# Kernel tuning notes

Measured on AMD Instinct MI355X. Metric: run time of the kernel, lower is better.

The kernel has to match this reference:

```python
import jax, jax.numpy as jnp
import numpy as np

B, L, D = 512, 200, 128
N_ITEMS = 50001
T_STEPS = 4
TAU = 2.0
STEP = 1
V_TH = 1.0
SG_ALPHA = 4.0  # spikingjelly default surrogate.Sigmoid alpha


@jax.custom_vjp
def spike(x):
    return (x >= 0.0).astype(x.dtype)

def _spike_fwd(x):
    return spike(x), x

def _spike_bwd(x, g):
    s = jax.nn.sigmoid(SG_ALPHA * x)
    return (g * SG_ALPHA * s * (1.0 - s),)

spike.defvjp(_spike_fwd, _spike_bwd)


def lif_multistep(x):
    """Multi-step LIF (hard reset to 0, detach_reset). x: [T, ...] -> spikes [T, ...]."""
    def step(v, xt):
        v = v + (xt - v) / TAU  # charge (v_reset = 0)
        s = spike(v - V_TH)
        v = v - jax.lax.stop_gradient(s) * v  # hard reset, detached spike
        return v, s
    v0 = jnp.zeros_like(x[0])
    _, spikes = jax.lax.scan(step, v0, x)
    return spikes


def layernorm(x, g, b, eps=1e-5):
    m = x.mean(-1, keepdims=True)
    v = x.var(-1, keepdims=True)
    return (x - m) / jnp.sqrt(v + eps) * g + b


def _build_session_graphs(rng):
    lens = rng.integers(50, L + 1, size=B)
    item_seq = np.zeros((B, L), dtype=np.int64)
    for b in range(B):
        item_seq[b, :lens[b]] = rng.integers(1, N_ITEMS, size=lens[b])
    alias = np.zeros((B, L), dtype=np.int64)
    items = np.zeros((B, L), dtype=np.int64)
    A = np.zeros((B, L, 2 * L), dtype=np.float32)
    for b in range(B):
        u = item_seq[b]
        node = np.unique(u)  # sorted
        items[b, :len(node)] = node
        alias[b] = np.searchsorted(node, u)
        uA = np.zeros((L, L), dtype=np.float32)
        for i in range(L - 1):
            if u[i + 1] == 0:
                break
            r = np.searchsorted(node, u[i])
            c = np.searchsorted(node, u[i + 1])
            uA[r, c] = 1.0
        sin = uA.sum(0); sin[sin == 0] = 1.0
        sout = uA.sum(1); sout[sout == 0] = 1.0
        A[b, :, :L] = (uA / sin).T          # u_A_in.T
        A[b, :, L:] = ((uA.T / sout)).T     # u_A_out.T
    mask = item_seq > 0
    return A, alias, items, mask, lens.astype(np.int64)


def setup_inputs() -> dict:
    rng = np.random.default_rng(0)
    A, alias, items, mask, lens = _build_session_graphs(rng)
    stdv = 1.0 / np.sqrt(D)
    key = jax.random.key(0)
    ks = jax.random.split(key, 24)
    u = lambda k, shape: jax.random.uniform(k, shape, jnp.float32, -stdv, stdv)
    item_emb = u(ks[0], (N_ITEMS, D)).at[0].set(0.0)  # padding_idx=0
    return {
        "A": jnp.asarray(A),
        "alias_inputs": jnp.asarray(alias),
        "items": jnp.asarray(items),
        "mask": jnp.asarray(mask),
        "item_seq_len": jnp.asarray(lens),
        "item_emb": item_emb,
        "W_in": u(ks[1], (D, D)), "b_in": u(ks[2], (D,)),
        "W_out": u(ks[3], (D, D)), "b_out": u(ks[4], (D,)),
        "w_ih": u(ks[5], (3 * D, 2 * D)), "w_hh": u(ks[6], (3 * D, D)),
        "b_ih": u(ks[7], (3 * D,)), "b_hh": u(ks[8], (3 * D,)),
        "b_iah": u(ks[9], (D,)), "b_ioh": u(ks[10], (D,)),
        "W1": u(ks[11], (D, D)), "W2": u(ks[12], (D, D)),
        "W3": u(ks[13], (1, D)), "Wt": u(ks[14], (D, 2 * D)),
        "g_q": u(ks[15], (D,)), "beta_q": u(ks[16], (D,)),
        "g_sh": u(ks[17], (2 * D,)), "beta_sh": u(ks[18], (2 * D,)),
    }


def _forward(A, alias_inputs, items, mask, item_seq_len, item_emb,
             W_in, b_in, W_out, b_out, w_ih, w_hh, b_ih, b_hh, b_iah, b_ioh,
             W1, W2, W3, Wt, g_q, beta_q, g_sh, beta_sh):
    hidden = item_emb[items]  # [B,L,D]
    for _ in range(STEP):
        ein = hidden @ W_in.T + b_in
        eout = hidden @ W_out.T + b_out
        input_in = jnp.einsum('bij,bjd->bid', A[:, :, :L], ein) + b_iah
        input_out = jnp.einsum('bij,bjd->bid', A[:, :, L:], eout) + b_ioh
        inputs = jnp.concatenate([input_in, input_out], axis=-1)  # [B,L,2D]
        gi = inputs @ w_ih.T + b_ih  # [B,L,3D]
        gh = hidden @ w_hh.T + b_hh
        i_r, i_i, i_n = jnp.split(gi, 3, axis=-1)
        h_r, h_i, h_n = jnp.split(gh, 3, axis=-1)
        r = jax.nn.sigmoid(i_r + h_r)
        z = jax.nn.sigmoid(i_i + h_i)
        n = jnp.tanh(i_n + r * h_n)
        hidden = (1.0 - z) * hidden + z * n
    seq_hidden = jnp.take_along_axis(hidden, alias_inputs[..., None], axis=1)  # [B,L,D]
    ht = jnp.take_along_axis(seq_hidden, (item_seq_len - 1)[:, None, None], axis=1)[:, 0]  # [B,D]
    Qb = (ht @ W1.T)[:, None, :] + seq_hidden @ W2.T  # [B,L,D]
    Q = jnp.broadcast_to(Qb[None], (T_STEPS, B, L, D))
    Qs = lif_multistep(layernorm(Q, g_q, beta_q))
    alpha = Qs @ W3.T  # [T,B,L,1]
    mf = mask.astype(alpha.dtype)
    a = jnp.sum(alpha * seq_hidden[None] * mf[None, :, :, None], axis=2)  # [T,B,D]
    ht_T = jnp.broadcast_to(ht[None], (T_STEPS, B, D))
    sh = jnp.concatenate([a, ht_T], axis=-1)  # [T,B,2D]
    sh = layernorm(lif_multistep(sh), g_sh, beta_sh)
    return (sh @ Wt.T).mean(0)  # [B,D]


def reference(A, alias_inputs, items, mask, item_seq_len, item_emb,
              W_in, b_in, W_out, b_out, w_ih, w_hh, b_ih, b_hh, b_iah, b_ioh,
              W1, W2, W3, Wt, g_q, beta_q, g_sh, beta_sh):
    return _forward(A, alias_inputs, items, mask, item_seq_len, item_emb,
                    W_in, b_in, W_out, b_out, w_ih, w_hh, b_ih, b_hh, b_iah, b_ioh,
                    W1, W2, W3, Wt, g_q, beta_q, g_sh, beta_sh)
```

## Files before the change

### kernel.cpp

```cpp
#include <hip/hip_runtime.h>
#include <hip/hip_bf16.h>
#include <cstdint>
#include <cstddef>

#define B_ 512
#define L_ 200
#define D_ 128
#define M_ (B_*L_)
#define T_ 4

typedef short bf16x8 __attribute__((ext_vector_type(8)));
typedef unsigned short u16x8 __attribute__((ext_vector_type(8)));
typedef float f32x4 __attribute__((ext_vector_type(4)));

__device__ __forceinline__ float bf2f(unsigned short u){
  union { unsigned int i; float f; } c; c.i = ((unsigned int)u)<<16; return c.f;
}
__device__ __forceinline__ unsigned short f2bf(float f){
  union { float f; unsigned int i; } c; c.f = f;
  unsigned int r = c.i + 0x7FFFu + ((c.i>>16)&1u);
  return (unsigned short)(r>>16);
}
__device__ __forceinline__ float wsum(float v){
  #pragma unroll
  for (int m=1;m<64;m<<=1) v += __shfl_xor(v, m, 64);
  return v;
}
__device__ __forceinline__ void gload_lds16(const void* g, void* l){
  __builtin_amdgcn_global_load_lds(
      (const __attribute__((address_space(1))) void*)g,
      (__attribute__((address_space(3))) void*)l, 16, 0, 0);
}

__global__ __launch_bounds__(256)
void gemm_bt(const unsigned short* __restrict__ A, int lda,
             const unsigned short* __restrict__ Bt, int ldb,
             const float* __restrict__ bias,
             unsigned short* __restrict__ C, int ldc, int K,
             const int* __restrict__ mlimit)
{
  const int m0 = blockIdx.y * 128;
  if (mlimit && m0 >= *mlimit) return;
  __shared__ __align__(16) short sAs[2][128*32];
  __shared__ __align__(16) short sBs[2][128*32];
  const int tid = threadIdx.x;
  const int n0 = blockIdx.x * 128;
  const int lane = tid & 63;
  const int w = tid >> 6;
  const int wr = (w>>1)*64, wc = (w&1)*64;

  f32x4 acc[4][4];
  #pragma unroll
  for (int i=0;i<4;i++)
    #pragma unroll
    for (int j=0;j<4;j++) acc[i][j] = (f32x4){0.f,0.f,0.f,0.f};

  const int c1 = tid, c2 = tid + 256;
  const int r1 = c1>>2, s1 = c1&3, k1 = ((s1 ^ ((r1>>1)&3))&3)<<3;
  const int r2 = c2>>2, s2 = c2&3, k2 = ((s2 ^ ((r2>>1)&3))&3)<<3;
  const int fr = lane & 15;
  const int fq = lane >> 4;
  const int fk = ((fq ^ ((fr>>1)&3))&3)<<3;

  auto stage = [&](int t){
    const int buf = t & 1, ks = t << 5;
    gload_lds16(A  + (size_t)(m0 + r1)*lda + ks + k1, sAs[buf] + (size_t)c1*8);
    gload_lds16(A  + (size_t)(m0 + r2)*lda + ks + k2, sAs[buf] + (size_t)c2*8);
    gload_lds16(Bt + (size_t)(n0 + r1)*ldb + ks + k1, sBs[buf] + (size_t)c1*8);
    gload_lds16(Bt + (size_t)(n0 + r2)*ldb + ks + k2, sBs[buf] + (size_t)c2*8);
  };
  const int nT = K >> 5;
  stage(0);
  __syncthreads();
  for (int t=0; t<nT; ++t){
    if (t+1 < nT) stage(t+1);
    const short* a_ = sAs[t&1];
    const short* b_ = sBs[t&1];
    bf16x8 af[4], bfr[4];
    #pragma unroll
    for (int i=0;i<4;i++){
      af[i]  = *(const bf16x8*)(a_ + (wr + i*16 + fr)*32 + fk);
      bfr[i] = *(const bf16x8*)(b_ + (wc + i*16 + fr)*32 + fk);
    }
    #pragma unroll
    for (int i=0;i<4;i++)
      #pragma unroll
      for (int j=0;j<4;j++)
        acc[i][j] = __builtin_amdgcn_mfma_f32_16x16x32_bf16(af[i], bfr[j], acc[i][j], 0,0,0);
    __syncthreads();
  }

  const int orow = fq<<2;
  #pragma unroll
  for (int i=0;i<4;i++){
    #pragma unroll
    for (int j=0;j<4;j++){
      const int gn = n0 + wc + j*16 + fr;
      const float bv = bias ? bias[gn] : 0.f;
      #pragma unroll
      for (int v=0;v<4;v++){
        const int gm = m0 + wr + i*16 + orow + v;
        C[(size_t)gm*ldc + gn] = f2bf(acc[i][j][v] + bv);
      }
    }
  }
}

__global__ __launch_bounds__(128)
void k_prepW(const float* __restrict__ w_ih, const float* __restrict__ w_hh,
             const float* __restrict__ W_in, const float* __restrict__ W_out,
             const float* __restrict__ b_in, const float* __restrict__ b_out,
             const float* __restrict__ b_ih, const float* __restrict__ b_hh,
             const float* __restrict__ b_iah, const float* __restrict__ b_ioh,
             const float* __restrict__ W2,
             unsigned short* __restrict__ Wbig, float* __restrict__ biasBase,
             float* __restrict__ uIn, float* __restrict__ uOut,
             unsigned short* __restrict__ w2b)
{
  const int p = blockIdx.x, t = threadIdx.x;
  if (p < 128) w2b[p*128 + t] = f2bf(W2[p*128 + t]);
  const int dim = p>>2, g = p&3;
  const int row = (g==0) ? dim : (g==1) ? 128+dim : 256+dim;
  const bool has_ih = (g!=3), has_hh = (g!=2);
  __shared__ float wl[128], wrg[128], red[3][128];
  wl[t]  = has_ih ? w_ih[(size_t)row*256 + t]       : 0.f;
  wrg[t] = has_ih ? w_ih[(size_t)row*256 + 128 + t] : 0.f;
  __syncthreads();
  float cin = 0.f, cout = 0.f;
  if (has_ih) {
    for (int m=0;m<128;m++){
      cin  += wl[m]  * W_in [m*128 + t];
      cout += wrg[m] * W_out[m*128 + t];
    }
  }
  Wbig[(size_t)p*384 +       t] = f2bf(cin);
  Wbig[(size_t)p*384 + 128 + t] = f2bf(cout);
  Wbig[(size_t)p*384 + 256 + t] = f2bf(has_hh ? w_hh[(size_t)row*128 + t] : 0.f);
  red[0][t] = wl[t]*b_iah[t] + wrg[t]*b_ioh[t];
  red[1][t] = wl[t]*b_in[t];
  red[2][t] = wrg[t]*b_out[t];
  __syncthreads();
  if (t == 0) {
    float v=0.f, ui=0.f, uo=0.f;
    for (int k=0;k<128;k++){ v += red[0][k]; ui += red[1][k]; uo += red[2][k]; }
    float bb;
    if (g==0)      bb = b_ih[dim]     + b_hh[dim]     + v;
    else if (g==1) bb = b_ih[128+dim] + b_hh[128+dim] + v;
    else if (g==2) bb = b_ih[256+dim] + v;
    else           bb = b_hh[256+dim];
    biasBase[p] = bb;
    uIn[p]  = has_ih ? ui : 0.f;
    uOut[p] = has_ih ? uo : 0.f;
  }
}

__global__ __launch_bounds__(64)
void k_nb(const int* __restrict__ alias, const int* __restrict__ lens,
          int* __restrict__ nb)
{
  const int b = blockIdx.x, lane = threadIdx.x;
  const int len = lens[b];
  int m = 0;
  for (int l=lane; l<len; l+=64) m = max(m, alias[b*L_ + l]);
  #pragma unroll
  for (int o=1;o<64;o<<=1) m = max(m, __shfl_xor(m, o, 64));
  if (lane==0) nb[b] = m + 1;
}

__global__ __launch_bounds__(512)
void k_scan(const int* __restrict__ nb, const int* __restrict__ lens,
            int* __restrict__ nbase, int* __restrict__ vbase)
{
  __shared__ int A[2][512], Bv[2][512];
  const int t = threadIdx.x;
  const int a0 = nb[t], b0 = lens[t];
  A[0][t] = a0; Bv[0][t] = b0;
  __syncthreads();
  int cur = 0;
  for (int off=1; off<512; off<<=1){
    const int nxt = cur^1;
    A[nxt][t]  = A[cur][t]  + (t>=off ? A[cur][t-off]  : 0);
    Bv[nxt][t] = Bv[cur][t] + (t>=off ? Bv[cur][t-off] : 0);
    __syncthreads();
    cur = nxt;
  }
  nbase[t] = A[cur][t] - a0;
  vbase[t] = Bv[cur][t] - b0;
  if (t==511){ nbase[512] = A[cur][511]; vbase[512] = Bv[cur][511]; }
}

__global__ __launch_bounds__(1024)
void k_aggemb(const int* __restrict__ alias, const int* __restrict__ items,
              const int* __restrict__ lens, const float* __restrict__ emb,
              const int* __restrict__ nb, const int* __restrict__ nbase,
              unsigned short* __restrict__ X3, unsigned char* __restrict__ cf)
{
  const int b = blockIdx.x, tid = threadIdx.x;
  __shared__ unsigned short hl[L_*128];
  __shared__ int al[L_], it[L_];
  __shared__ unsigned bmIn[L_*8], bmOut[L_*8];
  if (tid < L_) { al[tid] = alias[b*L_ + tid]; it[tid] = items[b*L_ + tid]; }
  for (int i=tid; i<L_*8; i+=1024){ bmIn[i]=0u; bmOut[i]=0u; }
  __syncthreads();
  const int len = lens[b], nB = nb[b], base = nbase[b];
  if (tid < len-1) {
    const int r = al[tid], c = al[tid+1];
    atomicOr(&bmIn[c*8 + (r>>5)],  1u<<(r&31));
    atomicOr(&bmOut[r*8 + (c>>5)], 1u<<(c&31));
  }
  const int rr = tid>>5, cc = (tid&31)<<2;
  for (int s=0; s<nB; s+=32) {
    const int j = s + rr;
    if (j < nB) {
      const float4 v = *(const float4*)(emb + (size_t)it[j]*128 + cc);
      ushort4 o; o.x=f2bf(v.x); o.y=f2bf(v.y); o.z=f2bf(v.z); o.w=f2bf(v.w);
      *(ushort4*)(hl + j*128 + cc) = o;
      *(ushort4*)(X3 + (size_t)(base + j)*384 + 256 + cc) = o;
    }
  }
  __syncthreads();
  const int g = tid >> 7, d = tid & 127;
  for (int s=0; s<nB; s+=8) {
    const int i = s + g;
    if (i < nB) {
      float si=0.f, so=0.f; int ci=0, co=0;
      #pragma unroll
      for (int wd=0; wd<8; ++wd) {
        unsigned word = bmIn[i*8+wd];
        while (word) { int j = __ffs(word)-1; word &= word-1u;
          si += bf2f(hl[(wd*32+j)*128 + d]); ci++; }
        word = bmOut[i*8+wd];
        while (word) { int j = __ffs(word)-1; word &= word-1u;
          so += bf2f(hl[(wd*32+j)*128 + d]); co++; }
      }
      unsigned short* xr = X3 + (size_t)(base + i)*384;
      xr[d]       = f2bf(si / (float)(ci>0?ci:1));
      xr[128 + d] = f2bf(so / (float)(co>0?co:1));
      if (d == 0) cf[base + i] = (unsigned char)((ci>0?1:0) | (co>0?2:0));
    }
  }
}

__global__ __launch_bounds__(512)
void k_gates_gru(const unsigned short* __restrict__ X3,
                 const unsigned short* __restrict__ Wbig,
                 const float* __restrict__ biasBase,
                 const float* __restrict__ uIn,
                 const float* __restrict__ uOut,
                 const unsigned char* __restrict__ cf,
                 unsigned short* __restrict__ hidden,
                 const int* __restrict__ mlimit)
{
  const int m0 = blockIdx.y * 128;
  if (m0 >= *mlimit) return;
  __shared__ __align__(16) short sA[2][128*32];
  __shared__ __align__(16) short sB[2][256*32];
  const int tid = threadIdx.x;
  const int p0 = blockIdx.x * 256;
  const int lane = tid & 63;
  const int w = tid >> 6;
  const int wr  = (w>>2)*64;
  const int wcp = (w&3)*64;
  const int fr = lane & 15;
  const int fq = lane >> 4;
  const int fk = ((fq ^ ((fr>>1)&3))&3)<<3;

  f32x4 acc[4][4];
  #pragma unroll
  for (int i=0;i<4;i++)
    #pragma unroll
    for (int j=0;j<4;j++) acc[i][j] = (f32x4){0.f,0.f,0.f,0.f};

  const int ra = tid>>2, sa_ = tid&3, ka = ((sa_ ^ ((ra>>1)&3))&3)<<3;
  const int c1 = tid + 512, rb1 = c1>>2, sb1 = c1&3, kb1 = ((sb1 ^ ((rb1>>1)&3))&3)<<3;

  auto stage = [&](int t){
    const int buf = t & 1, ks = t << 5;
    gload_lds16(X3   + (size_t)(m0 + ra )*384 + ks + ka , sA[buf] + (size_t)tid*8);
    gload_lds16(Wbig + (size_t)(p0 + ra )*384 + ks + ka , sB[buf] + (size_t)tid*8);
    gload_lds16(Wbig + (size_t)(p0 + rb1)*384 + ks + kb1, sB[buf] + (size_t)(c1-512)*8 + 512*8);
  };
  stage(0);
  __syncthreads();
  for (int t=0; t<12; ++t){
    if (t < 11) stage(t+1);
    const short* a_ = sA[t&1];
    const short* b_ = sB[t&1];
    bf16x8 af[4], bfr[4];
    #pragma unroll
    for (int i=0;i<4;i++){
      af[i]  = *(const bf16x8*)(a_ + (wr  + i*16 + fr)*32 + fk);
      bfr[i] = *(const bf16x8*)(b_ + (wcp + i*16 + fr)*32 + fk);
    }
    #pragma unroll
    for (int i=0;i<4;i++)
      #pragma unroll
      for (int j=0;j<4;j++)
        acc[i][j] = __builtin_amdgcn_mfma_f32_16x16x32_bf16(af[i], bfr[j], acc[i][j], 0,0,0);
    __syncthreads();
  }

  const bool q0b = (lane & 1), q1b = (lane & 2);
  #pragma unroll
  for (int j=0;j<4;j++){
    const int dim = (p0>>2) + (w&3)*16 + j*4 + ((lane>>2)&3);
    const float4 bb = *(const float4*)(biasBase + dim*4);
    const float4 bi = *(const float4*)(uIn  + dim*4);
    const float4 bo = *(const float4*)(uOut + dim*4);
    #pragma unroll
    for (int i=0;i<4;i++){
      const float a0=acc[i][j][0], a1=acc[i][j][1], a2=acc[i][j][2], a3=acc[i][j][3];
      const float t0=__shfl_xor(a0,1), t1=__shfl_xor(a1,1), t2=__shfl_xor(a2,1), t3=__shfl_xor(a3,1);
      const float s0 = q0b? t1:a0, s1 = q0b? a1:t0, s2 = q0b? t3:a2, s3 = q0b? a3:t2;
      const float u0=__shfl_xor(s0,2), u1=__shfl_xor(s1,2), u2=__shfl_xor(s2,2), u3=__shfl_xor(s3,2);
      float G0 = q1b? u2:s0, G1 = q1b? u3:s1, G2 = q1b? s2:u0, G3 = q1b? s3:u1;
      const int row = m0 + wr + i*16 + fq*4 + (lane&3);
      const unsigned c = cf[row];
      const float fi = (c&1) ? 1.f : 0.f, fo = (c&2) ? 1.f : 0.f;
      G0 += bb.x + fi*bi.x + fo*bo.x;
      G1 += bb.y + fi*bi.y + fo*bo.y;
      G2 += bb.z + fi*bi.z + fo*bo.z;
      G3 += bb.w;
      const float h = bf2f(X3[(size_t)row*384 + 256 + dim]);
      const float r = 1.f/(1.f+__expf(-G0));
      const float z = 1.f/(1.f+__expf(-G1));
      const float x = G2 + r*G3;
      const float n = 1.f - 2.f/(__expf(2.f*x)+1.f);
      hidden[(size_t)row*128 + dim] = f2bf((1.f-z)*h + z*n);
    }
  }
}

__global__ __launch_bounds__(256)
void k_gather(const unsigned short* __restrict__ hidden,
              const int* __restrict__ alias, const int* __restrict__ lens,
              const int* __restrict__ nbase, const int* __restrict__ vbase,
              unsigned short* __restrict__ seqv)
{
  const int idx = blockIdx.x*256 + threadIdx.x;
  const int row = idx >> 4, d8 = (idx & 15) << 3;
  const int b = row / L_, l = row - b*L_;
  const int len = lens[b];
  if (l >= len) return;
  const int vrow = vbase[b] + l;
  u16x8 v = *(const u16x8*)(hidden + (size_t)(nbase[b] + alias[row])*128 + d8);
  *(u16x8*)(seqv + (size_t)vrow*128 + d8) = v;
}

__global__ __launch_bounds__(1024)
void k_attn(const unsigned short* __restrict__ Q0,
            const unsigned short* __restrict__ seqv, const int* __restrict__ lens,
            const int* __restrict__ vbase, const float* __restrict__ W1,
            const float* __restrict__ g_q, const float* __restrict__ beta_q,
            const float* __restrict__ W3, float* __restrict__ a_out)
{
  const int b = blockIdx.x, tid = threadIdx.x;
  const int w = tid>>6, lane = tid&63;
  __shared__ float a_acc[16][T_][128];
  __shared__ float htv[128], htw[128];
  const int len = lens[b], vb = vbase[b];
  for (int i=tid; i<16*T_*128; i+=1024) ((float*)a_acc)[i] = 0.f;
  if (tid < 128) htv[tid] = bf2f(seqv[(size_t)(vb + len - 1)*128 + tid]);
  __syncthreads();
  {
    const int d = tid >> 3, seg = (tid & 7) << 4;
    const float* wr1 = W1 + (size_t)d*128 + seg;
    const float* hv = htv + seg;
    float p = 0.f;
    #pragma unroll
    for (int k=0;k<16;k++) p += wr1[k]*hv[k];
    p += __shfl_xor(p, 1, 64); p += __shfl_xor(p, 2, 64); p += __shfl_xor(p, 4, 64);
    if ((tid & 7) == 0) htw[d] = p;
  }
  __syncthreads();
  const float h0 = htw[lane], h1 = htw[lane+64];
  const float gq0 = g_q[lane], gq1 = g_q[lane+64];
  const float bq0 = beta_q[lane], bq1 = beta_q[lane+64];
  const float w30 = W3[lane], w31 = W3[lane+64];
  for (int l = w; l < len; l += 16) {
    const size_t row = (size_t)(vb + l);
    const float q0 = bf2f(Q0[row*128 + lane]) + h0;
    const float q1 = bf2f(Q0[row*128 + lane + 64]) + h1;
    const float m = wsum(q0+q1) * (1.f/128.f);
    const float d0 = q0-m, d1 = q1-m;
    const float var = wsum(d0*d0 + d1*d1) * (1.f/128.f);
    const float inv = rsqrtf(var + 1e-5f);
    const float x0 = d0*inv*gq0 + bq0;
    const float x1 = d1*inv*gq1 + bq1;
    const float sh0 = bf2f(seqv[row*128+lane]), sh1 = bf2f(seqv[row*128+lane+64]);
    float v0=0.f, v1=0.f;
    #pragma unroll
    for (int t=0;t<T_;t++){
      v0 = 0.5f*(v0+x0); v1 = 0.5f*(v1+x1);
      const float s0 = (v0>=1.f)?1.f:0.f, s1 = (v1>=1.f)?1.f:0.f;
      v0 -= s0*v0; v1 -= s1*v1;
      const float alpha = wsum(s0*w30 + s1*w31);
      a_acc[w][t][lane] += alpha*sh0; a_acc[w][t][lane+64] += alpha*sh1;
    }
  }
  __syncthreads();
  for (int i=tid; i<T_*128; i+=1024){
    const int t = i>>7, d = i&127;
    float s = 0.f;
    #pragma unroll
    for (int p=0;p<16;p++) s += a_acc[p][t][d];
    a_out[((size_t)t*B_ + b)*128 + d] = s;
  }
}

__global__ __launch_bounds__(256)
void k_final(const float* __restrict__ a_in, const unsigned short* __restrict__ hidden,
             const int* __restrict__ alias, const int* __restrict__ lens,
             const int* __restrict__ nbase,
             const float* __restrict__ g_sh, const float* __restrict__ beta_sh,
             const float* __restrict__ Wt, float* __restrict__ out)
{
  const int b = blockIdx.x, tid = threadIdx.x;
  const int w = tid>>6, lane = tid&63;
  __shared__ float ys[256];
  __shared__ float part[T_][4];
  const int len = lens[b];
  float xh = 0.f;
  if (tid >= 128) {
    const int al = alias[b*L_ + len - 1];
    xh = bf2f(hidden[((size_t)(nbase[b] + al))*128 + (tid-128)]);
  }
  float v = 0.f; float sp[T_];
  #pragma unroll
  for (int t=0;t<T_;t++){
    const float x = (tid<128) ? a_in[((size_t)t*B_ + b)*128 + tid] : xh;
    v = 0.5f*(v + x);
    const float s = (v>=1.f)?1.f:0.f;
    v -= s*v;
    sp[t] = s;
  }
  #pragma unroll
  for (int t=0;t<T_;t++){
    const float r = wsum(sp[t]);
    if (lane==0) part[t][w] = r;
  }
  __syncthreads();
  float acc4 = 0.f;
  #pragma unroll
  for (int t=0;t<T_;t++){
    const float k = part[t][0]+part[t][1]+part[t][2]+part[t][3];
    const float mean = k * (1.f/256.f);
    const float varr = mean - mean*mean;
    const float inv = rsqrtf(varr + 1e-5f);
    acc4 += (sp[t]-mean)*inv;
  }
  ys[tid] = acc4*g_sh[tid] + 4.f*beta_sh[tid];
  __syncthreads();
  if (tid < 128) {
    float acc = 0.f;
    const float4* wr4 = (const float4*)(Wt + (size_t)tid*256);
    const float4* ys4 = (const float4*)ys;
    #pragma unroll 8
    for (int k=0;k<64;k++){
      const float4 wv = wr4[k], yv = ys4[k];
      acc += wv.x*yv.x + wv.y*yv.y + wv.z*yv.z + wv.w*yv.w;
    }
    out[(size_t)b*128 + tid] = acc*0.25f;
  }
}

extern "C" void kernel_launch(void* const* d_in, const int* in_sizes, int n_in,
                              void* d_out, int out_size, void* d_ws, size_t ws_size,
                              hipStream_t stream)
{
  const int*   alias  = (const int*)d_in[1];
  const int*   items  = (const int*)d_in[2];
  const int*   lens   = (const int*)d_in[4];
  const float* emb    = (const float*)d_in[5];
  const float* W_in   = (const float*)d_in[6];
  const float* b_in   = (const float*)d_in[7];
  const float* W_out  = (const float*)d_in[8];
  const float* b_out  = (const float*)d_in[9];
  const float* w_ih   = (const float*)d_in[10];
  const float* w_hh   = (const float*)d_in[11];
  const float* b_ih   = (const float*)d_in[12];
  const float* b_hh   = (const float*)d_in[13];
  const float* b_iah  = (const float*)d_in[14];
  const float* b_ioh  = (const float*)d_in[15];
  const float* W1     = (const float*)d_in[16];
  const float* W2     = (const float*)d_in[17];
  const float* W3     = (const float*)d_in[18];
  const float* Wt     = (const float*)d_in[19];
  const float* g_q    = (const float*)d_in[20];
  const float* beta_q = (const float*)d_in[21];
  const float* g_sh   = (const float*)d_in[22];
  const float* beta_sh= (const float*)d_in[23];

  char* ws = (char*)d_ws;
  size_t off = 0;
  auto alloc = [&](size_t bytes)->void* {
    void* p = ws + off; off += (bytes + 255) & ~(size_t)255; return p;
  };
  unsigned short* X3    = (unsigned short*)alloc((size_t)M_*384*2);
  unsigned short* hidden= (unsigned short*)alloc((size_t)M_*128*2);
  unsigned short* seqv  = (unsigned short*)alloc((size_t)M_*128*2);
  unsigned short* Q0c   = (unsigned short*)alloc((size_t)M_*128*2);
  float*          a_buf = (float*)alloc((size_t)T_*B_*128*4);
  unsigned short* Wbig  = (unsigned short*)alloc((size_t)512*384*2);
  unsigned short* w2b   = (unsigned short*)alloc(16384*2);
  float*          biasBase = (float*)alloc(512*4);
  float*          uIn   = (float*)alloc(512*4);
  float*          uOut  = (float*)alloc(512*4);
  unsigned char*  cf    = (unsigned char*)alloc(M_);
  int*            nb    = (int*)alloc(512*4);
  int*            nbase = (int*)alloc(513*4);
  int*            vbase = (int*)alloc(513*4);
  if (off > ws_size) return;

  k_prepW<<<512,128,0,stream>>>(w_ih,w_hh,W_in,W_out,b_in,b_out,b_ih,b_hh,
                                b_iah,b_ioh,W2,Wbig,biasBase,uIn,uOut,w2b);
  k_nb<<<B_,64,0,stream>>>(alias, lens, nb);
  k_scan<<<1,512,0,stream>>>(nb, lens, nbase, vbase);
  k_aggemb<<<B_,1024,0,stream>>>(alias, items, lens, emb, nb, nbase, X3, cf);
  k_gates_gru<<<dim3(2,800),512,0,stream>>>(X3, Wbig, biasBase, uIn, uOut, cf,
                                            hidden, nbase+512);
  k_gather<<<M_*16/256,256,0,stream>>>(hidden, alias, lens, nbase, vbase, seqv);
  gemm_bt<<<dim3(1,800),256,0,stream>>>(seqv, 128, w2b, 128, nullptr, Q0c, 128, 128, vbase+512);
  k_attn<<<B_,1024,0,stream>>>(Q0c, seqv, lens, vbase, W1, g_q, beta_q, W3, a_buf);
  k_final<<<B_,256,0,stream>>>(a_buf, hidden, alias, lens, nbase, g_sh, beta_sh,
                               Wt, (float*)d_out);
}
```

Baseline: 191.8 us.

## Replace gather pass with index-driven loads and triple-buffer gates GEMM

Removes the k_gather kernel that copied hidden rows into a sequence-ordered buffer. A small k_gidx kernel now builds a row-index map, and the Q GEMM and attention kernels read hidden through that map directly, which drops one full write and re-read of the sequence buffer. The gates/GRU kernel moves to 256-thread 128x128 tiles with a three-stage LDS pipeline, using explicit vmcnt waits and one barrier per step in place of two syncs. The gathered GEMM loads may coalesce less well, and it adds an extra small launch.

Result: no change. 192.0 us (+0.1%).

```diff
diff --git a/kernel.cpp b/kernel.cpp
--- a/kernel.cpp
+++ b/kernel.cpp
@@ -37,10 +37,11 @@
              const unsigned short* __restrict__ Bt, int ldb,
              const float* __restrict__ bias,
              unsigned short* __restrict__ C, int ldc, int K,
-             const int* __restrict__ mlimit)
+             const int* __restrict__ mlimit, const int* __restrict__ gidx)
 {
   const int m0 = blockIdx.y * 128;
-  if (mlimit && m0 >= *mlimit) return;
+  const int Mv = mlimit ? *mlimit : (1<<30);
+  if (m0 >= Mv) return;
   __shared__ __align__(16) short sAs[2][128*32];
   __shared__ __align__(16) short sBs[2][128*32];
   const int tid = threadIdx.x;
@@ -58,14 +59,16 @@
   const int c1 = tid, c2 = tid + 256;
   const int r1 = c1>>2, s1 = c1&3, k1 = ((s1 ^ ((r1>>1)&3))&3)<<3;
   const int r2 = c2>>2, s2 = c2&3, k2 = ((s2 ^ ((r2>>1)&3))&3)<<3;
+  int ar1 = m0 + r1, ar2 = m0 + r2;
+  if (gidx){ ar1 = (ar1 < Mv) ? gidx[ar1] : 0; ar2 = (ar2 < Mv) ? gidx[ar2] : 0; }
   const int fr = lane & 15;
   const int fq = lane >> 4;
   const int fk = ((fq ^ ((fr>>1)&3))&3)<<3;
 
   auto stage = [&](int t){
     const int buf = t & 1, ks = t << 5;
-    gload_lds16(A  + (size_t)(m0 + r1)*lda + ks + k1, sAs[buf] + (size_t)c1*8);
-    gload_lds16(A  + (size_t)(m0 + r2)*lda + ks + k2, sAs[buf] + (size_t)c2*8);
+    gload_lds16(A  + (size_t)ar1*lda + ks + k1, sAs[buf] + (size_t)c1*8);
+    gload_lds16(A  + (size_t)ar2*lda + ks + k2, sAs[buf] + (size_t)c2*8);
     gload_lds16(Bt + (size_t)(n0 + r1)*ldb + ks + k1, sBs[buf] + (size_t)c1*8);
     gload_lds16(Bt + (size_t)(n0 + r2)*ldb + ks + k2, sBs[buf] + (size_t)c2*8);
   };
@@ -187,6 +190,16 @@
   nbase[t] = A[cur][t] - a0;
   vbase[t] = Bv[cur][t] - b0;
   if (t==511){ nbase[512] = A[cur][511]; vbase[512] = Bv[cur][511]; }
+}
+
+__global__ __launch_bounds__(256)
+void k_gidx(const int* __restrict__ alias, const int* __restrict__ lens,
+            const int* __restrict__ nbase, const int* __restrict__ vbase,
+            int* __restrict__ gidx)
+{
+  const int idx = blockIdx.x*256 + threadIdx.x;
+  const int b = idx / L_, l = idx - b*L_;
+  if (l < lens[b]) gidx[vbase[b]+l] = nbase[b] + alias[idx];
 }
 
 __global__ __launch_bounds__(1024)
@@ -241,7 +254,7 @@
   }
 }
 
-__global__ __launch_bounds__(512)
+__global__ __launch_bounds__(256)
 void k_gates_gru(const unsigned short* __restrict__ X3,
                  const unsigned short* __restrict__ Wbig,
                  const float* __restrict__ biasBase,
@@ -253,14 +266,13 @@
 {
   const int m0 = blockIdx.y * 128;
   if (m0 >= *mlimit) return;
-  __shared__ __align__(16) short sA[2][128*32];
-  __shared__ __align__(16) short sB[2][256*32];
+  __shared__ __align__(16) short sA[3][128*32];
+  __shared__ __align__(16) short sB[3][128*32];
   const int tid = threadIdx.x;
-  const int p0 = blockIdx.x * 256;
+  const int p0 = blockIdx.x * 128;
   const int lane = tid & 63;
   const int w = tid >> 6;
-  const int wr  = (w>>2)*64;
-  const int wcp = (w&3)*64;
+  const int wr = (w>>1)*64, wc = (w&1)*64;
   const int fr = lane & 15;
   const int fq = lane >> 4;
   const int fk = ((fq ^ ((fr>>1)&3))&3)<<3;
@@ -271,39 +283,43 @@
     #pragma unroll
     for (int j=0;j<4;j++) acc[i][j] = (f32x4){0.f,0.f,0.f,0.f};
 
-  const int ra = tid>>2, sa_ = tid&3, ka = ((sa_ ^ ((ra>>1)&3))&3)<<3;
-  const int c1 = tid + 512, rb1 = c1>>2, sb1 = c1&3, kb1 = ((sb1 ^ ((rb1>>1)&3))&3)<<3;
+  const int c1 = tid, c2 = tid + 256;
+  const int r1 = c1>>2, s1 = c1&3, k1 = ((s1 ^ ((r1>>1)&3))&3)<<3;
+  const int r2 = c2>>2, s2 = c2&3, k2 = ((s2 ^ ((r2>>1)&3))&3)<<3;
 
   auto stage = [&](int t){
-    const int buf = t & 1, ks = t << 5;
-    gload_lds16(X3   + (size_t)(m0 + ra )*384 + ks + ka , sA[buf] + (size_t)tid*8);
-    gload_lds16(Wbig + (size_t)(p0 + ra )*384 + ks + ka , sB[buf] + (size_t)tid*8);
-    gload_lds16(Wbig + (size_t)(p0 + rb1)*384 + ks + kb1, sB[buf] + (size_t)(c1-512)*8 + 512*8);
+    const int buf = t % 3, ks = t << 5;
+    gload_lds16(X3   + (size_t)(m0 + r1)*384 + ks + k1, sA[buf] + (size_t)c1*8);
+    gload_lds16(X3   + (size_t)(m0 + r2)*384 + ks + k2, sA[buf] + (size_t)c2*8);
+    gload_lds16(Wbig + (size_t)(p0 + r1)*384 + ks + k1, sB[buf] + (size_t)c1*8);
+    gload_lds16(Wbig + (size_t)(p0 + r2)*384 + ks + k2, sB[buf] + (size_t)c2*8);
   };
-  stage(0);
-  __syncthreads();
+  stage(0); stage(1);
   for (int t=0; t<12; ++t){
-    if (t < 11) stage(t+1);
-    const short* a_ = sA[t&1];
-    const short* b_ = sB[t&1];
+    if (t < 11) { asm volatile("s_waitcnt vmcnt(4)" ::: "memory"); }
+    else        { asm volatile("s_waitcnt vmcnt(0)" ::: "memory"); }
+    __builtin_amdgcn_s_barrier();
+    if (t+2 < 12) stage(t+2);
+    const short* a_ = sA[t%3];
+    const short* b_ = sB[t%3];
     bf16x8 af[4], bfr[4];
     #pragma unroll
     for (int i=0;i<4;i++){
-      af[i]  = *(const bf16x8*)(a_ + (wr  + i*16 + fr)*32 + fk);
-      bfr[i] = *(const bf16x8*)(b_ + (wcp + i*16 + fr)*32 + fk);
+      af[i]  = *(const bf16x8*)(a_ + (wr + i*16 + fr)*32 + fk);
+      bfr[i] = *(const bf16x8*)(b_ + (wc + i*16 + fr)*32 + fk);
     }
     #pragma unroll
     for (int i=0;i<4;i++)
       #pragma unroll
       for (int j=0;j<4;j++)
         acc[i][j] = __builtin_amdgcn_mfma_f32_16x16x32_bf16(af[i], bfr[j], acc[i][j], 0,0,0);
-    __syncthreads();
-  }
+  }
+  __builtin_amdgcn_s_barrier();
 
   const bool q0b = (lane & 1), q1b = (lane & 2);
   #pragma unroll
   for (int j=0;j<4;j++){
-    const int dim = (p0>>2) + (w&3)*16 + j*4 + ((lane>>2)&3);
+    const int dim = (p0>>2) + (w&1)*16 + j*4 + ((lane>>2)&3);
     const float4 bb = *(const float4*)(biasBase + dim*4);
     const float4 bi = *(const float4*)(uIn  + dim*4);
     const float4 bo = *(const float4*)(uOut + dim*4);
@@ -331,26 +347,11 @@
   }
 }
 
-__global__ __launch_bounds__(256)
-void k_gather(const unsigned short* __restrict__ hidden,
-              const int* __restrict__ alias, const int* __restrict__ lens,
-              const int* __restrict__ nbase, const int* __restrict__ vbase,
-              unsigned short* __restrict__ seqv)
-{
-  const int idx = blockIdx.x*256 + threadIdx.x;
-  const int row = idx >> 4, d8 = (idx & 15) << 3;
-  const int b = row / L_, l = row - b*L_;
-  const int len = lens[b];
-  if (l >= len) return;
-  const int vrow = vbase[b] + l;
-  u16x8 v = *(const u16x8*)(hidden + (size_t)(nbase[b] + alias[row])*128 + d8);
-  *(u16x8*)(seqv + (size_t)vrow*128 + d8) = v;
-}
-
 __global__ __launch_bounds__(1024)
 void k_attn(const unsigned short* __restrict__ Q0,
-            const unsigned short* __restrict__ seqv, const int* __restrict__ lens,
-            const int* __restrict__ vbase, const float* __restrict__ W1,
+            const unsigned short* __restrict__ hidden, const int* __restrict__ gidx,
+            const int* __restrict__ lens, const int* __restrict__ vbase,
+            const float* __restrict__ W1,
             const float* __restrict__ g_q, const float* __restrict__ beta_q,
             const float* __restrict__ W3, float* __restrict__ a_out)
 {
@@ -360,7 +361,7 @@
   __shared__ float htv[128], htw[128];
   const int len = lens[b], vb = vbase[b];
   for (int i=tid; i<16*T_*128; i+=1024) ((float*)a_acc)[i] = 0.f;
-  if (tid < 128) htv[tid] = bf2f(seqv[(size_t)(vb + len - 1)*128 + tid]);
+  if (tid < 128) htv[tid] = bf2f(hidden[(size_t)gidx[vb + len - 1]*128 + tid]);
   __syncthreads();
   {
     const int d = tid >> 3, seg = (tid & 7) << 4;
@@ -379,6 +380,7 @@
   const float w30 = W3[lane], w31 = W3[lane+64];
   for (int l = w; l < len; l += 16) {
     const size_t row = (size_t)(vb + l);
+    const size_t hrow = (size_t)gidx[row];
     const float q0 = bf2f(Q0[row*128 + lane]) + h0;
     const float q1 = bf2f(Q0[row*128 + lane + 64]) + h1;
     const float m = wsum(q0+q1) * (1.f/128.f);
@@ -387,7 +389,7 @@
     const float inv = rsqrtf(var + 1e-5f);
     const float x0 = d0*inv*gq0 + bq0;
     const float x1 = d1*inv*gq1 + bq1;
-    const float sh0 = bf2f(seqv[row*128+lane]), sh1 = bf2f(seqv[row*128+lane+64]);
+    const float sh0 = bf2f(hidden[hrow*128+lane]), sh1 = bf2f(hidden[hrow*128+lane+64]);
     float v0=0.f, v1=0.f;
     #pragma unroll
     for (int t=0;t<T_;t++){
@@ -498,8 +500,8 @@
   };
   unsigned short* X3    = (unsigned short*)alloc((size_t)M_*384*2);
   unsigned short* hidden= (unsigned short*)alloc((size_t)M_*128*2);
-  unsigned short* seqv  = (unsigned short*)alloc((size_t)M_*128*2);
   unsigned short* Q0c   = (unsigned short*)alloc((size_t)M_*128*2);
+  int*            gidx  = (int*)alloc((size_t)M_*4);
   float*          a_buf = (float*)alloc((size_t)T_*B_*128*4);
   unsigned short* Wbig  = (unsigned short*)alloc((size_t)512*384*2);
   unsigned short* w2b   = (unsigned short*)alloc(16384*2);
@@ -516,12 +518,14 @@
                                 b_iah,b_ioh,W2,Wbig,biasBase,uIn,uOut,w2b);
   k_nb<<<B_,64,0,stream>>>(alias, lens, nb);
   k_scan<<<1,512,0,stream>>>(nb, lens, nbase, vbase);
+  k_gidx<<<M_/256,256,0,stream>>>(alias, lens, nbase, vbase, gidx);
   k_aggemb<<<B_,1024,0,stream>>>(alias, items, lens, emb, nb, nbase, X3, cf);
-  k_gates_gru<<<dim3(2,800),512,0,stream>>>(X3, Wbig, biasBase, uIn, uOut, cf,
+  k_gates_gru<<<dim3(4,800),256,0,stream>>>(X3, Wbig, biasBase, uIn, uOut, cf,
                                             hidden, nbase+512);
-  k_gather<<<M_*16/256,256,0,stream>>>(hidden, alias, lens, nbase, vbase, seqv);
-  gemm_bt<<<dim3(1,800),256,0,stream>>>(seqv, 128, w2b, 128, nullptr, Q0c, 128, 128, vbase+512);
-  k_attn<<<B_,1024,0,stream>>>(Q0c, seqv, lens, vbase, W1, g_q, beta_q, W3, a_buf);
+  gemm_bt<<<dim3(1,800),256,0,stream>>>(hidden, 128, w2b, 128, nullptr, Q0c, 128,
+                                        128, vbase+512, gidx);
+  k_attn<<<B_,1024,0,stream>>>(Q0c, hidden, gidx, lens, vbase, W1, g_q, beta_q,
+                               W3, a_buf);
   k_final<<<B_,256,0,stream>>>(a_buf, hidden, alias, lens, nbase, g_sh, beta_sh,
                                Wt, (float*)d_out);
 }
```

## Fold gather into GEMM via row index and fuse final stage into attention

Applied to the files above, without the earlier changes.

Removes the k_gather kernel and the seqv buffer. The Q GEMM and the attention kernel now read hidden rows indirectly through a gidx map that k_aggemb writes. The k_final kernel is merged into k_attn, so the per-step attention sums stay in shared memory instead of round-tripping through global memory. This saves two launches and one full-size copy, at the cost of indirect, less coalesced row loads in the GEMM and attention kernels.

New measurement: 180.0 us. -6.1%, faster.

```diff
diff --git a/kernel.cpp b/kernel.cpp
--- a/kernel.cpp
+++ b/kernel.cpp
@@ -37,10 +37,11 @@
              const unsigned short* __restrict__ Bt, int ldb,
              const float* __restrict__ bias,
              unsigned short* __restrict__ C, int ldc, int K,
-             const int* __restrict__ mlimit)
+             const int* __restrict__ mlimit, const int* __restrict__ gidx)
 {
   const int m0 = blockIdx.y * 128;
-  if (mlimit && m0 >= *mlimit) return;
+  const int Mv = mlimit ? *mlimit : (1<<30);
+  if (m0 >= Mv) return;
   __shared__ __align__(16) short sAs[2][128*32];
   __shared__ __align__(16) short sBs[2][128*32];
   const int tid = threadIdx.x;
@@ -58,14 +59,16 @@
   const int c1 = tid, c2 = tid + 256;
   const int r1 = c1>>2, s1 = c1&3, k1 = ((s1 ^ ((r1>>1)&3))&3)<<3;
   const int r2 = c2>>2, s2 = c2&3, k2 = ((s2 ^ ((r2>>1)&3))&3)<<3;
+  int ar1 = m0 + r1, ar2 = m0 + r2;
+  if (gidx){ ar1 = (ar1 < Mv) ? gidx[ar1] : 0; ar2 = (ar2 < Mv) ? gidx[ar2] : 0; }
   const int fr = lane & 15;
   const int fq = lane >> 4;
   const int fk = ((fq ^ ((fr>>1)&3))&3)<<3;
 
   auto stage = [&](int t){
     const int buf = t & 1, ks = t << 5;
-    gload_lds16(A  + (size_t)(m0 + r1)*lda + ks + k1, sAs[buf] + (size_t)c1*8);
-    gload_lds16(A  + (size_t)(m0 + r2)*lda + ks + k2, sAs[buf] + (size_t)c2*8);
+    gload_lds16(A  + (size_t)ar1*lda + ks + k1, sAs[buf] + (size_t)c1*8);
+    gload_lds16(A  + (size_t)ar2*lda + ks + k2, sAs[buf] + (size_t)c2*8);
     gload_lds16(Bt + (size_t)(n0 + r1)*ldb + ks + k1, sBs[buf] + (size_t)c1*8);
     gload_lds16(Bt + (size_t)(n0 + r2)*ldb + ks + k2, sBs[buf] + (size_t)c2*8);
   };
@@ -193,7 +196,9 @@
 void k_aggemb(const int* __restrict__ alias, const int* __restrict__ items,
               const int* __restrict__ lens, const float* __restrict__ emb,
               const int* __restrict__ nb, const int* __restrict__ nbase,
-              unsigned short* __restrict__ X3, unsigned char* __restrict__ cf)
+              const int* __restrict__ vbase,
+              unsigned short* __restrict__ X3, unsigned char* __restrict__ cf,
+              int* __restrict__ gidx)
 {
   const int b = blockIdx.x, tid = threadIdx.x;
   __shared__ unsigned short hl[L_*128];
@@ -203,6 +208,7 @@
   for (int i=tid; i<L_*8; i+=1024){ bmIn[i]=0u; bmOut[i]=0u; }
   __syncthreads();
   const int len = lens[b], nB = nb[b], base = nbase[b];
+  if (tid < len) gidx[vbase[b] + tid] = base + al[tid];
   if (tid < len-1) {
     const int r = al[tid], c = al[tid+1];
     atomicOr(&bmIn[c*8 + (r>>5)],  1u<<(r&31));
@@ -331,36 +337,25 @@
   }
 }
 
-__global__ __launch_bounds__(256)
-void k_gather(const unsigned short* __restrict__ hidden,
-              const int* __restrict__ alias, const int* __restrict__ lens,
-              const int* __restrict__ nbase, const int* __restrict__ vbase,
-              unsigned short* __restrict__ seqv)
-{
-  const int idx = blockIdx.x*256 + threadIdx.x;
-  const int row = idx >> 4, d8 = (idx & 15) << 3;
-  const int b = row / L_, l = row - b*L_;
-  const int len = lens[b];
-  if (l >= len) return;
-  const int vrow = vbase[b] + l;
-  u16x8 v = *(const u16x8*)(hidden + (size_t)(nbase[b] + alias[row])*128 + d8);
-  *(u16x8*)(seqv + (size_t)vrow*128 + d8) = v;
-}
-
 __global__ __launch_bounds__(1024)
 void k_attn(const unsigned short* __restrict__ Q0,
-            const unsigned short* __restrict__ seqv, const int* __restrict__ lens,
-            const int* __restrict__ vbase, const float* __restrict__ W1,
+            const unsigned short* __restrict__ hidden, const int* __restrict__ gidx,
+            const int* __restrict__ lens, const int* __restrict__ vbase,
+            const float* __restrict__ W1,
             const float* __restrict__ g_q, const float* __restrict__ beta_q,
-            const float* __restrict__ W3, float* __restrict__ a_out)
+            const float* __restrict__ W3,
+            const float* __restrict__ g_sh, const float* __restrict__ beta_sh,
+            const float* __restrict__ Wt, float* __restrict__ out)
 {
   const int b = blockIdx.x, tid = threadIdx.x;
   const int w = tid>>6, lane = tid&63;
   __shared__ float a_acc[16][T_][128];
   __shared__ float htv[128], htw[128];
+  __shared__ float ys[256];
+  __shared__ float part[T_][4];
   const int len = lens[b], vb = vbase[b];
   for (int i=tid; i<16*T_*128; i+=1024) ((float*)a_acc)[i] = 0.f;
-  if (tid < 128) htv[tid] = bf2f(seqv[(size_t)(vb + len - 1)*128 + tid]);
+  if (tid < 128) htv[tid] = bf2f(hidden[(size_t)gidx[vb + len - 1]*128 + tid]);
   __syncthreads();
   {
     const int d = tid >> 3, seg = (tid & 7) << 4;
@@ -379,6 +374,7 @@
   const float w30 = W3[lane], w31 = W3[lane+64];
   for (int l = w; l < len; l += 16) {
     const size_t row = (size_t)(vb + l);
+    const size_t hrow = (size_t)gidx[row];
     const float q0 = bf2f(Q0[row*128 + lane]) + h0;
     const float q1 = bf2f(Q0[row*128 + lane + 64]) + h1;
     const float m = wsum(q0+q1) * (1.f/128.f);
@@ -387,7 +383,7 @@
     const float inv = rsqrtf(var + 1e-5f);
     const float x0 = d0*inv*gq0 + bq0;
     const float x1 = d1*inv*gq1 + bq1;
-    const float sh0 = bf2f(seqv[row*128+lane]), sh1 = bf2f(seqv[row*128+lane+64]);
+    const float sh0 = bf2f(hidden[hrow*128+lane]), sh1 = bf2f(hidden[hrow*128+lane+64]);
     float v0=0.f, v1=0.f;
     #pragma unroll
     for (int t=0;t<T_;t++){
@@ -399,57 +395,43 @@
     }
   }
   __syncthreads();
-  for (int i=tid; i<T_*128; i+=1024){
-    const int t = i>>7, d = i&127;
-    float s = 0.f;
-    #pragma unroll
-    for (int p=0;p<16;p++) s += a_acc[p][t][d];
-    a_out[((size_t)t*B_ + b)*128 + d] = s;
-  }
-}
-
-__global__ __launch_bounds__(256)
-void k_final(const float* __restrict__ a_in, const unsigned short* __restrict__ hidden,
-             const int* __restrict__ alias, const int* __restrict__ lens,
-             const int* __restrict__ nbase,
-             const float* __restrict__ g_sh, const float* __restrict__ beta_sh,
-             const float* __restrict__ Wt, float* __restrict__ out)
-{
-  const int b = blockIdx.x, tid = threadIdx.x;
-  const int w = tid>>6, lane = tid&63;
-  __shared__ float ys[256];
-  __shared__ float part[T_][4];
-  const int len = lens[b];
-  float xh = 0.f;
-  if (tid >= 128) {
-    const int al = alias[b*L_ + len - 1];
-    xh = bf2f(hidden[((size_t)(nbase[b] + al))*128 + (tid-128)]);
-  }
-  float v = 0.f; float sp[T_];
-  #pragma unroll
-  for (int t=0;t<T_;t++){
-    const float x = (tid<128) ? a_in[((size_t)t*B_ + b)*128 + tid] : xh;
-    v = 0.5f*(v + x);
-    const float s = (v>=1.f)?1.f:0.f;
-    v -= s*v;
-    sp[t] = s;
-  }
-  #pragma unroll
-  for (int t=0;t<T_;t++){
-    const float r = wsum(sp[t]);
-    if (lane==0) part[t][w] = r;
-  }
-  __syncthreads();
-  float acc4 = 0.f;
-  #pragma unroll
-  for (int t=0;t<T_;t++){
-    const float k = part[t][0]+part[t][1]+part[t][2]+part[t][3];
-    const float mean = k * (1.f/256.f);
-    const float varr = mean - mean*mean;
-    const float inv = rsqrtf(varr + 1e-5f);
-    acc4 += (sp[t]-mean)*inv;
-  }
-  ys[tid] = acc4*g_sh[tid] + 4.f*beta_sh[tid];
+
+  float sp[T_] = {0.f,0.f,0.f,0.f};
+  if (tid < 256) {
+    const float xh = (tid >= 128) ? htv[tid-128] : 0.f;
+    float v = 0.f;
+    #pragma unroll
+    for (int t=0;t<T_;t++){
+      float x;
+      if (tid < 128) {
+        x = 0.f;
+        #pragma unroll
+        for (int p=0;p<16;p++) x += a_acc[p][t][tid];
+      } else x = xh;
+      v = 0.5f*(v + x);
+      const float s = (v>=1.f)?1.f:0.f;
+      v -= s*v;
+      sp[t] = s;
+    }
+    #pragma unroll
+    for (int t=0;t<T_;t++){
+      const float r = wsum(sp[t]);
+      if (lane==0) part[t][w] = r;
+    }
+  }
+  __syncthreads();
+  if (tid < 256) {
+    float acc4 = 0.f;
+    #pragma unroll
+    for (int t=0;t<T_;t++){
+      const float k = part[t][0]+part[t][1]+part[t][2]+part[t][3];
+      const float mean = k * (1.f/256.f);
+      const float varr = mean - mean*mean;
+      const float inv = rsqrtf(varr + 1e-5f);
+      acc4 += (sp[t]-mean)*inv;
+    }
+    ys[tid] = acc4*g_sh[tid] + 4.f*beta_sh[tid];
+  }
   __syncthreads();
   if (tid < 128) {
     float acc = 0.f;
@@ -498,9 +480,8 @@
   };
   unsigned short* X3    = (unsigned short*)alloc((size_t)M_*384*2);
   unsigned short* hidden= (unsigned short*)alloc((size_t)M_*128*2);
-  unsigned short* seqv  = (unsigned short*)alloc((size_t)M_*128*2);
   unsigned short* Q0c   = (unsigned short*)alloc((size_t)M_*128*2);
-  float*          a_buf = (float*)alloc((size_t)T_*B_*128*4);
+  int*            gidx  = (int*)alloc((size_t)M_*4);
   unsigned short* Wbig  = (unsigned short*)alloc((size_t)512*384*2);
   unsigned short* w2b   = (unsigned short*)alloc(16384*2);
   float*          biasBase = (float*)alloc(512*4);
@@ -516,12 +497,12 @@
                                 b_iah,b_ioh,W2,Wbig,biasBase,uIn,uOut,w2b);
   k_nb<<<B_,64,0,stream>>>(alias, lens, nb);
   k_scan<<<1,512,0,stream>>>(nb, lens, nbase, vbase);
-  k_aggemb<<<B_,1024,0,stream>>>(alias, items, lens, emb, nb, nbase, X3, cf);
+  k_aggemb<<<B_,1024,0,stream>>>(alias, items, lens, emb, nb, nbase, vbase,
+                                 X3, cf, gidx);
   k_gates_gru<<<dim3(2,800),512,0,stream>>>(X3, Wbig, biasBase, uIn, uOut, cf,
                                             hidden, nbase+512);
-  k_gather<<<M_*16/256,256,0,stream>>>(hidden, alias, lens, nbase, vbase, seqv);
-  gemm_bt<<<dim3(1,800),256,0,stream>>>(seqv, 128, w2b, 128, nullptr, Q0c, 128, 128, vbase+512);
-  k_attn<<<B_,1024,0,stream>>>(Q0c, seqv, lens, vbase, W1, g_q, beta_q, W3, a_buf);
-  k_final<<<B_,256,0,stream>>>(a_buf, hidden, alias, lens, nbase, g_sh, beta_sh,
-                               Wt, (float*)d_out);
-}
+  gemm_bt<<<dim3(1,800),256,0,stream>>>(hidden, 128, w2b, 128, nullptr, Q0c, 128,
+                                        128, vbase+512, gidx);
+  k_attn<<<B_,1024,0,stream>>>(Q0c, hidden, gidx, lens, vbase, W1, g_q, beta_q,
+                               W3, g_sh, beta_sh, Wt, (float*)d_out);
+}
```
